# Kernel tuning notes

Measured on AMD Instinct MI355X. Metric: run time of the kernel, lower is better.

Reference implementation:

```python
import jax, jax.numpy as jnp
import numpy as np
from jax import lax

NUM_HEADS = 8
EMBED_DIM = 256
KEY_DIM = EMBED_DIM // NUM_HEADS  # 32


def rotate_every_two(x):
    x1 = x[..., ::2]
    x2 = x[..., 1::2]
    return jnp.stack((-x2, x1), axis=-1).reshape(x.shape)


def theta_shift(x, sin, cos):
    return x * cos + rotate_every_two(x) * sin


def setup_inputs() -> dict:
    key = jax.random.key(0)
    ks = jax.random.split(key, 16)
    b, H, W, E = 16, 64, 64, EMBED_DIM
    kd = KEY_DIM
    gain = 2 ** (-2.5)
    std_proj = gain * (2.0 / (E + E)) ** 0.5  # xavier_normal with gain
    std_out = (2.0 / (E + E)) ** 0.5
    return {
        "x": jax.random.normal(ks[0], (b, H, W, E), jnp.float32),
        "sin": jax.random.normal(ks[1], (H, W, kd), jnp.float32),
        "cos": jax.random.normal(ks[2], (H, W, kd), jnp.float32),
        "mask_h": jax.random.normal(ks[3], (NUM_HEADS, H, H), jnp.float32),
        "mask_w": jax.random.normal(ks[4], (NUM_HEADS, W, W), jnp.float32),
        "q_w": jax.random.normal(ks[5], (E, E), jnp.float32) * std_proj,
        "q_b": jnp.zeros((E,), jnp.float32),
        "k_w": jax.random.normal(ks[6], (E, E), jnp.float32) * std_proj,
        "k_b": jnp.zeros((E,), jnp.float32),
        "v_w": jax.random.normal(ks[7], (E, E), jnp.float32) * std_proj,
        "v_b": jnp.zeros((E,), jnp.float32),
        "lepe_w": jax.random.normal(ks[8], (5, 5, 1, E), jnp.float32) * 0.05,  # HWIO depthwise
        "lepe_b": jnp.zeros((E,), jnp.float32),
        "out_w": jax.random.normal(ks[9], (E, E), jnp.float32) * std_out,
        "out_b": jnp.zeros((E,), jnp.float32),
    }


def reference(x, sin, cos, mask_h, mask_w, q_w, q_b, k_w, k_b, v_w, v_b,
              lepe_w, lepe_b, out_w, out_b):
    b, H, W, E = x.shape
    nH, kd = NUM_HEADS, KEY_DIM
    vd = E // nH
    scaling = kd ** (-0.5)

    q = x @ q_w + q_b                       # [b,H,W,E]
    k = (x @ k_w + k_b) * scaling
    v = x @ v_w + v_b

    # depthwise 5x5 conv (lepe), NHWC
    lepe = lax.conv_general_dilated(
        v, lepe_w, window_strides=(1, 1), padding=[(2, 2), (2, 2)],
        dimension_numbers=("NHWC", "HWIO", "NHWC"), feature_group_count=E) + lepe_b

    q = q.reshape(b, H, W, nH, kd)
    k = k.reshape(b, H, W, nH, kd)
    v = v.reshape(b, H, W, nH, vd)

    sin_b = sin[:, :, None, :]              # [H,W,1,kd]
    cos_b = cos[:, :, None, :]
    qr = theta_shift(q, sin_b, cos_b)       # [b,H,W,nH,kd]
    kr = theta_shift(k, sin_b, cos_b)

    # width-wise attention: scores [b,H,nH,W,W]
    qk_w = jnp.einsum("bhqnd,bhknd->bhnqk", qr, kr)
    attn_w = jax.nn.softmax(qk_w + mask_w[None, None], axis=-1)
    v1 = jnp.einsum("bhnqk,bhknd->bhqnd", attn_w, v)  # [b,H,W,nH,vd]

    # height-wise attention: scores [b,W,nH,H,H]
    qk_h = jnp.einsum("bqwnd,bkwnd->bwnqk", qr, kr)
    attn_h = jax.nn.softmax(qk_h + mask_h[None, None], axis=-1)
    out = jnp.einsum("bwnqk,bkwnd->bqwnd", attn_h, v1)  # [b,H,W,nH,vd]

    out = out.reshape(b, H, W, E) + lepe
    return out @ out_w + out_b
```

## Files before the change

kernel.cpp:

```cpp
#include <hip/hip_runtime.h>

typedef unsigned short u16;
typedef __attribute__((ext_vector_type(4))) float f32x4;
typedef __attribute__((ext_vector_type(8))) short bf16x8;
typedef __attribute__((ext_vector_type(8))) u16 u16x8;
typedef __attribute__((ext_vector_type(4))) u16 u16x4v;

#define DI __device__ __forceinline__

DI u16 f2bf(float f) {
  unsigned int x = __float_as_uint(f);
  unsigned int r = (x + 0x7fffu + ((x >> 16) & 1u)) >> 16;
  return (u16)r;
}
DI float bf2f(u16 u) { return __uint_as_float(((unsigned int)u) << 16); }

__global__ __launch_bounds__(256) void pack_kernel(
    const float* __restrict__ qw, const float* __restrict__ qb,
    const float* __restrict__ kw, const float* __restrict__ kb,
    const float* __restrict__ vw, const float* __restrict__ vb,
    const float* __restrict__ ow,
    u16* __restrict__ wqkvT, float* __restrict__ bias, u16* __restrict__ owT)
{
  const int r = blockIdx.x;
  const int t = threadIdx.x;
  if (r < 768) {
    const int p = r >> 8, c = r & 255;
    const float* wsrc = p == 0 ? qw : (p == 1 ? kw : vw);
    const float sc = (p == 1) ? 0.17677669529663687f : 1.0f;
    wqkvT[r * 256 + t] = f2bf(wsrc[t * 256 + c] * sc);
    if (t == 0) {
      const float* bs = p == 0 ? qb : (p == 1 ? kb : vb);
      bias[r] = bs[c] * sc;
    }
  } else {
    const int c = r - 768;
    owT[c * 256 + t] = f2bf(ow[t * 256 + c]);
  }
}

__global__ __launch_bounds__(256, 2) void qkv_gemm_kernel(
    const float* __restrict__ x, const u16* __restrict__ wT, const float* __restrict__ bias,
    const float* __restrict__ sinp, const float* __restrict__ cosp,
    u16* __restrict__ qr, u16* __restrict__ kr, u16* __restrict__ v)
{
  __shared__ u16 As[32768];
  __shared__ float Tr[4][1024];
  const int t = threadIdx.x;
  const int wave = t >> 6, lane = t & 63;
  const int g = lane >> 4, lr = lane & 15;
  const int wr = wave >> 1, wc = wave & 1;
  const int m0 = blockIdx.x * 128;

  {
    char* Abw = (char*)As;
#pragma unroll
    for (int i = 0; i < 32; ++i) {
      const int c = t + 256 * i;
      const int row = c >> 6, cf = c & 63;
      const float4 xv = *reinterpret_cast<const float4*>(x + (m0 + row) * 256 + cf * 4);
      u16x4v bv;
      bv.x = f2bf(xv.x); bv.y = f2bf(xv.y); bv.z = f2bf(xv.z); bv.w = f2bf(xv.w);
      *reinterpret_cast<u16x4v*>(Abw + row * 512 + ((cf * 8) ^ ((row & 7) << 4))) = bv;
    }
  }
  __syncthreads();

  const char* Ab = (const char*)As;
  float* Trw = Tr[wave];
  const int tau = lane >> 3;
  const int kap = lane & 7;

  for (int cg = 0; cg < 6; ++cg) {
    const int c0 = cg * 128;
    f32x4 acc[4][4];
#pragma unroll
    for (int i = 0; i < 4; ++i)
#pragma unroll
      for (int j = 0; j < 4; ++j) acc[i][j] = (f32x4){0.f, 0.f, 0.f, 0.f};

#pragma unroll
    for (int ks = 0; ks < 8; ++ks) {
      bf16x8 af[4], bfr[4];
#pragma unroll
      for (int mt = 0; mt < 4; ++mt) {
        const int rr = wr * 64 + mt * 16 + lr;
        const int cb = (ks * 64 + g * 16) ^ ((rr & 7) << 4);
        af[mt] = *reinterpret_cast<const bf16x8*>(Ab + rr * 512 + cb);
      }
#pragma unroll
      for (int nt = 0; nt < 4; ++nt)
        bfr[nt] = *reinterpret_cast<const bf16x8*>(wT + (c0 + wc * 64 + nt * 16 + lr) * 256 + ks * 32 + g * 8);
#pragma unroll
      for (int mt = 0; mt < 4; ++mt)
#pragma unroll
        for (int nt = 0; nt < 4; ++nt)
          acc[mt][nt] = __builtin_amdgcn_mfma_f32_16x16x32_bf16(af[mt], bfr[nt], acc[mt][nt], 0, 0, 0);
    }

    const int colb = c0 + wc * 64;
    const int proj = colb >> 8;
    u16* dst = proj == 0 ? qr : (proj == 1 ? kr : v);
    const int e0 = (colb & 255) + kap * 8;

    float bcv[4];
#pragma unroll
    for (int nt = 0; nt < 4; ++nt) bcv[nt] = bias[colb + nt * 16 + lr];

#pragma unroll
    for (int mt = 0; mt < 4; ++mt) {
#pragma unroll
      for (int nt = 0; nt < 4; ++nt)
#pragma unroll
        for (int j = 0; j < 4; ++j)
          Trw[(g * 4 + j) * 64 + ((nt * 16 + lr) ^ (8 * j) ^ (16 * (g & 1)))] =
              acc[mt][nt][j] + bcv[nt];
      asm volatile("s_waitcnt lgkmcnt(0)" ::: "memory");
#pragma unroll
      for (int r2 = 0; r2 < 2; ++r2) {
        const int row = tau + 8 * r2;
        const int sig = (8 * (row & 3)) ^ (16 * ((row >> 2) & 1));
        const int rb = row * 64 + ((kap * 8) ^ sig);
        const float4 v0 = *reinterpret_cast<const float4*>(Trw + rb);
        const float4 v1 = *reinterpret_cast<const float4*>(Trw + rb + 4);
        const int tok = m0 + wr * 64 + mt * 16 + row;
        u16x8 o;
        if (proj < 2) {
          const int pos = tok & 4095;
          const int d0 = (kap * 8) & 31;
          const float* sp2 = sinp + pos * 32 + d0;
          const float* cp2 = cosp + pos * 32 + d0;
          {
            const float4 s0 = *reinterpret_cast<const float4*>(sp2);
            const float4 cA = *reinterpret_cast<const float4*>(cp2);
            o[0] = f2bf(v0.x * cA.x - v0.y * s0.x);
            o[1] = f2bf(v0.y * cA.y + v0.x * s0.y);
            o[2] = f2bf(v0.z * cA.z - v0.w * s0.z);
            o[3] = f2bf(v0.w * cA.w + v0.z * s0.w);
          }
          {
            const float4 s1 = *reinterpret_cast<const float4*>(sp2 + 4);
            const float4 cB = *reinterpret_cast<const float4*>(cp2 + 4);
            o[4] = f2bf(v1.x * cB.x - v1.y * s1.x);
            o[5] = f2bf(v1.y * cB.y + v1.x * s1.y);
            o[6] = f2bf(v1.z * cB.z - v1.w * s1.z);
            o[7] = f2bf(v1.w * cB.w + v1.z * s1.w);
          }
        } else {
          o[0] = f2bf(v0.x); o[1] = f2bf(v0.y); o[2] = f2bf(v0.z); o[3] = f2bf(v0.w);
          o[4] = f2bf(v1.x); o[5] = f2bf(v1.y); o[6] = f2bf(v1.z); o[7] = f2bf(v1.w);
        }
        *reinterpret_cast<u16x8*>(dst + tok * 256 + e0) = o;
      }
      asm volatile("s_waitcnt lgkmcnt(0)" ::: "memory");
    }
  }
}

__global__ __launch_bounds__(256, 2) void attn_kernel(
    const u16* __restrict__ qr, const u16* __restrict__ kr, const u16* __restrict__ vsrc,
    const float* __restrict__ mask, u16* __restrict__ dst, const int mode)
{
  __shared__ u16 Pbuf[4][64][72];
  __shared__ u16 Vt[256][80];
  const int t = threadIdx.x;
  const int wave = t >> 6, lane = t & 63;
  const int g = lane >> 4, lr = lane & 15;
  const int b = blockIdx.x >> 6, o = blockIdx.x & 63;
  const int base = (mode == 0) ? (b * 4096 + o * 64) * 256 : (b * 4096 + o) * 256;
  const int ts = (mode == 0) ? 256 : 16384;

#pragma unroll
  for (int i = 0; i < 8; ++i) {
    const int c = t + 256 * i;
    const int tok = c >> 5, ch = c & 31;
    const u16x8 val = *reinterpret_cast<const u16x8*>(vsrc + base + tok * ts + ch * 8);
    const int tc = tok ^ ((ch & 7) * 8);
#pragma unroll
    for (int j = 0; j < 8; ++j) Vt[ch * 8 + j][tc] = val[j];
  }
  __syncthreads();

  u16x4v obf[2][4][2];

  for (int hh = 0; hh < 2; ++hh) {
    const int n = wave * 2 + hh;
    bf16x8 qf[4], kf[4];
#pragma unroll
    for (int mt = 0; mt < 4; ++mt) {
      qf[mt] = *reinterpret_cast<const bf16x8*>(qr + base + (mt * 16 + lr) * ts + n * 32 + g * 8);
      kf[mt] = *reinterpret_cast<const bf16x8*>(kr + base + (mt * 16 + lr) * ts + n * 32 + g * 8);
    }
    const f32x4 zero = (f32x4){0.f, 0.f, 0.f, 0.f};
    f32x4 s[4][4];
#pragma unroll
    for (int mt = 0; mt < 4; ++mt)
#pragma unroll
      for (int nt = 0; nt < 4; ++nt)
        s[mt][nt] = __builtin_amdgcn_mfma_f32_16x16x32_bf16(qf[mt], kf[nt], zero, 0, 0, 0);

    const float* mp = mask + n * 4096;
#pragma unroll
    for (int mt = 0; mt < 4; ++mt) {
#pragma unroll
      for (int j = 0; j < 4; ++j) {
        const int r = mt * 16 + g * 4 + j;
#pragma unroll
        for (int nt = 0; nt < 4; ++nt)
          s[mt][nt][j] += mp[r * 64 + nt * 16 + lr];
        float m = fmaxf(fmaxf(s[mt][0][j], s[mt][1][j]), fmaxf(s[mt][2][j], s[mt][3][j]));
        m = fmaxf(m, __shfl_xor(m, 1));
        m = fmaxf(m, __shfl_xor(m, 2));
        m = fmaxf(m, __shfl_xor(m, 4));
        m = fmaxf(m, __shfl_xor(m, 8));
        float sum = 0.f;
#pragma unroll
        for (int nt = 0; nt < 4; ++nt) {
          const float p = __expf(s[mt][nt][j] - m);
          s[mt][nt][j] = p;
          sum += p;
        }
        sum += __shfl_xor(sum, 1);
        sum += __shfl_xor(sum, 2);
        sum += __shfl_xor(sum, 4);
        sum += __shfl_xor(sum, 8);
        const float rs = 1.f / sum;
#pragma unroll
        for (int nt = 0; nt < 4; ++nt)
          Pbuf[wave][r][nt * 16 + lr] = f2bf(s[mt][nt][j] * rs);
      }
    }

    f32x4 oacc[4][2];
#pragma unroll
    for (int mt = 0; mt < 4; ++mt)
#pragma unroll
      for (int nd = 0; nd < 2; ++nd) oacc[mt][nd] = zero;

#pragma unroll
    for (int kt = 0; kt < 2; ++kt) {
      bf16x8 pa[4];
#pragma unroll
      for (int mt = 0; mt < 4; ++mt)
        pa[mt] = *reinterpret_cast<const bf16x8*>(&Pbuf[wave][mt * 16 + lr][kt * 32 + g * 8]);
#pragma unroll
      for (int nd = 0; nd < 2; ++nd) {
        const int dcol = n * 32 + nd * 16 + lr;
        const bf16x8 vb = *reinterpret_cast<const bf16x8*>(
            &Vt[dcol][(kt * 32 + g * 8) ^ (((dcol >> 3) & 7) * 8)]);
#pragma unroll
        for (int mt = 0; mt < 4; ++mt)
          oacc[mt][nd] = __builtin_amdgcn_mfma_f32_16x16x32_bf16(vb, pa[mt], oacc[mt][nd], 0, 0, 0);
      }
    }
#pragma unroll
    for (int mt = 0; mt < 4; ++mt)
#pragma unroll
      for (int nd = 0; nd < 2; ++nd) {
        obf[hh][mt][nd].x = f2bf(oacc[mt][nd][0]);
        obf[hh][mt][nd].y = f2bf(oacc[mt][nd][1]);
        obf[hh][mt][nd].z = f2bf(oacc[mt][nd][2]);
        obf[hh][mt][nd].w = f2bf(oacc[mt][nd][3]);
      }
  }

  u16* Pw = &Pbuf[wave][0][0];
#pragma unroll
  for (int hh = 0; hh < 2; ++hh)
#pragma unroll
    for (int mt = 0; mt < 4; ++mt)
#pragma unroll
      for (int nd = 0; nd < 2; ++nd)
        *reinterpret_cast<u16x4v*>(Pw + (mt * 16 + lr) * 72 + hh * 32 + nd * 16 + g * 4) =
            obf[hh][mt][nd];
  asm volatile("s_waitcnt lgkmcnt(0)" ::: "memory");
#pragma unroll
  for (int r = 0; r < 8; ++r) {
    const int tok = r * 8 + (lane >> 3);
    const int ch = (lane & 7) * 8;
    const u16x8 val = *reinterpret_cast<const u16x8*>(Pw + tok * 72 + ch);
    *reinterpret_cast<u16x8*>(dst + base + tok * ts + wave * 64 + ch) = val;
  }
}

__global__ __launch_bounds__(256) void lepe_kernel(
    const u16* __restrict__ v, const float* __restrict__ cw, const float* __restrict__ cb,
    u16* __restrict__ lepe)
{
  const int t = threadIdx.x;
  const int cg = t & 31, pg = t >> 5;
  const int c0 = cg * 8;
  const int rowi = blockIdx.x >> 1;
  const int w0 = (blockIdx.x & 1) * 32 + pg * 4;
  const int h = rowi & 63;

  float acc[4][8];
#pragma unroll
  for (int p = 0; p < 4; ++p)
#pragma unroll
    for (int j = 0; j < 8; ++j) acc[p][j] = 0.f;

#pragma unroll
  for (int dy = 0; dy < 5; ++dy) {
    const int hh = h + dy - 2;
    if ((unsigned)hh >= 64u) continue;
    const u16* vrow = v + (size_t)(rowi + dy - 2) * 64 * 256 + c0;
    float fin[8][8];
#pragma unroll
    for (int i = 0; i < 8; ++i) {
      const int ww = w0 - 2 + i;
      if ((unsigned)ww < 64u) {
        const u16x8 val = *reinterpret_cast<const u16x8*>(vrow + ww * 256);
#pragma unroll
        for (int j = 0; j < 8; ++j) fin[i][j] = bf2f(val[j]);
      } else {
#pragma unroll
        for (int j = 0; j < 8; ++j) fin[i][j] = 0.f;
      }
    }
#pragma unroll
    for (int dx = 0; dx < 5; ++dx) {
      const float* wp = cw + (dy * 5 + dx) * 256 + c0;
      const float4 wA = *reinterpret_cast<const float4*>(wp);
      const float4 wB = *reinterpret_cast<const float4*>(wp + 4);
      const float wv[8] = {wA.x, wA.y, wA.z, wA.w, wB.x, wB.y, wB.z, wB.w};
#pragma unroll
      for (int p = 0; p < 4; ++p)
#pragma unroll
        for (int j = 0; j < 8; ++j)
          acc[p][j] += fin[p + dx][j] * wv[j];
    }
  }

#pragma unroll
  for (int p = 0; p < 4; ++p) {
    u16x8 r;
#pragma unroll
    for (int j = 0; j < 8; ++j) r[j] = f2bf(acc[p][j] + cb[c0 + j]);
    *reinterpret_cast<u16x8*>(lepe + ((size_t)rowi * 64 + w0 + p) * 256 + c0) = r;
  }
}

__global__ __launch_bounds__(256, 2) void out_gemm_kernel(
    const u16* __restrict__ ao, const u16* __restrict__ lep, const u16* __restrict__ owT,
    const float* __restrict__ ob, float* __restrict__ out)
{
  __shared__ u16 As[16384];
  const int t = threadIdx.x;
  const int wave = t >> 6, lane = t & 63;
  const int g = lane >> 4, lr = lane & 15;
  const int m0 = blockIdx.x * 64;

  char* Abw = (char*)As;
#pragma unroll
  for (int i = 0; i < 8; ++i) {
    const int c = t + 256 * i;
    const int row = c >> 5, bc = (c & 31) << 4;
    const int off = (m0 + row) * 256 + (c & 31) * 8;
    const u16x8 a = *reinterpret_cast<const u16x8*>(ao + off);
    const u16x8 l = *reinterpret_cast<const u16x8*>(lep + off);
    u16x8 s;
#pragma unroll
    for (int j = 0; j < 8; ++j) s[j] = f2bf(bf2f(a[j]) + bf2f(l[j]));
    *reinterpret_cast<u16x8*>(Abw + row * 512 + (bc ^ ((row & 7) << 4))) = s;
  }
  __syncthreads();

  const char* Ab = (const char*)As;
  for (int cg = 0; cg < 2; ++cg) {
    const int c0w = cg * 128 + wave * 32;
    f32x4 acc[4][2];
#pragma unroll
    for (int i = 0; i < 4; ++i)
#pragma unroll
      for (int j = 0; j < 2; ++j) acc[i][j] = (f32x4){0.f, 0.f, 0.f, 0.f};

#pragma unroll
    for (int ks = 0; ks < 8; ++ks) {
      bf16x8 af[4];
#pragma unroll
      for (int mt = 0; mt < 4; ++mt) {
        const int rr = mt * 16 + lr;
        const int cb = (ks * 64 + g * 16) ^ ((rr & 7) << 4);
        af[mt] = *reinterpret_cast<const bf16x8*>(Ab + rr * 512 + cb);
      }
#pragma unroll
      for (int nt = 0; nt < 2; ++nt) {
        const bf16x8 b =
            *reinterpret_cast<const bf16x8*>(owT + (c0w + nt * 16 + lr) * 256 + ks * 32 + g * 8);
#pragma unroll
        for (int mt = 0; mt < 4; ++mt)
          acc[mt][nt] = __builtin_amdgcn_mfma_f32_16x16x32_bf16(b, af[mt], acc[mt][nt], 0, 0, 0);
      }
    }

#pragma unroll
    for (int mt = 0; mt < 4; ++mt) {
      const int tok = m0 + mt * 16 + lr;
#pragma unroll
      for (int nt = 0; nt < 2; ++nt) {
        const int col0 = c0w + nt * 16 + g * 4;
        const float4 ob4 = *reinterpret_cast<const float4*>(ob + col0);
        float4 o;
        o.x = acc[mt][nt][0] + ob4.x;
        o.y = acc[mt][nt][1] + ob4.y;
        o.z = acc[mt][nt][2] + ob4.z;
        o.w = acc[mt][nt][3] + ob4.w;
        *reinterpret_cast<float4*>(out + tok * 256 + col0) = o;
      }
    }
  }
}

extern "C" void kernel_launch(void* const* d_in, const int* in_sizes, int n_in,
                              void* d_out, int out_size, void* d_ws, size_t ws_size,
                              hipStream_t stream)
{
  const float* x      = (const float*)d_in[0];
  const float* sinp   = (const float*)d_in[1];
  const float* cosp   = (const float*)d_in[2];
  const float* mask_h = (const float*)d_in[3];
  const float* mask_w = (const float*)d_in[4];
  const float* q_w    = (const float*)d_in[5];
  const float* q_b    = (const float*)d_in[6];
  const float* k_w    = (const float*)d_in[7];
  const float* k_b    = (const float*)d_in[8];
  const float* v_w    = (const float*)d_in[9];
  const float* v_b    = (const float*)d_in[10];
  const float* lepe_w = (const float*)d_in[11];
  const float* lepe_b = (const float*)d_in[12];
  const float* out_w  = (const float*)d_in[13];
  const float* out_b  = (const float*)d_in[14];

  unsigned char* ws = (unsigned char*)d_ws;
  const size_t SZ = 33554432;
  u16* qr    = (u16*)(ws);
  u16* kr    = (u16*)(ws + SZ);
  u16* vv    = (u16*)(ws + 2 * SZ);
  u16* v1    = (u16*)(ws + 3 * SZ);
  u16* lepe  = (u16*)(ws + 4 * SZ);
  u16* wqkvT = (u16*)(ws + 5 * SZ);
  u16* owT   = (u16*)(ws + 5 * SZ + 393216);
  float* bias = (float*)(ws + 5 * SZ + 393216 + 131072);
  u16* attn_out = vv;

  pack_kernel<<<1024, 256, 0, stream>>>(q_w, q_b, k_w, k_b, v_w, v_b, out_w, wqkvT, bias, owT);
  qkv_gemm_kernel<<<512, 256, 0, stream>>>(x, wqkvT, bias, sinp, cosp, qr, kr, vv);
  lepe_kernel<<<2048, 256, 0, stream>>>(vv, lepe_w, lepe_b, lepe);
  attn_kernel<<<1024, 256, 0, stream>>>(qr, kr, vv, mask_w, v1, 0);
  attn_kernel<<<1024, 256, 0, stream>>>(qr, kr, v1, mask_h, attn_out, 1);
  out_gemm_kernel<<<1024, 256, 0, stream>>>(attn_out, lepe, owT, out_b, (float*)d_out);
}
```

Baseline: 281.7 us.

## Compute transposed attention scores and pass probabilities via shuffles instead of LDS

The attention kernel now computes S^T (keys as rows) one 16-query tile at a time. Each query's softmax then reduces over a single lane column with two cross-lane shuffles, and the bf16 probabilities go straight into the P·V MFMA through 64-bit lane shuffles, so the per-wave LDS probability buffer is gone. The masks are pre-transposed in the pack kernel to match the new layout. The output staging reuses the V tile's shared memory with an XOR swizzle after a barrier, and launch bounds rise to 3 blocks per SU for more occupancy. The cost is extra shuffle instructions and more register pressure under the tighter bound.

```diff
diff --git a/kernel.cpp b/kernel.cpp
--- a/kernel.cpp
+++ b/kernel.cpp
@@ -1,10 +1,12 @@
 #include <hip/hip_runtime.h>
 
 typedef unsigned short u16;
+typedef unsigned long long u64;
 typedef __attribute__((ext_vector_type(4))) float f32x4;
 typedef __attribute__((ext_vector_type(8))) short bf16x8;
 typedef __attribute__((ext_vector_type(8))) u16 u16x8;
 typedef __attribute__((ext_vector_type(4))) u16 u16x4v;
+typedef __attribute__((ext_vector_type(2))) u64 u64x2;
 
 #define DI __device__ __forceinline__
 
@@ -14,13 +16,20 @@
   return (u16)r;
 }
 DI float bf2f(u16 u) { return __uint_as_float(((unsigned int)u) << 16); }
+DI u64 shfl64(u64 v, int src) {
+  int lo = __shfl((int)(unsigned int)(v & 0xffffffffu), src, 64);
+  int hi = __shfl((int)(unsigned int)(v >> 32), src, 64);
+  return ((u64)(unsigned int)hi << 32) | (u64)(unsigned int)lo;
+}
 
 __global__ __launch_bounds__(256) void pack_kernel(
     const float* __restrict__ qw, const float* __restrict__ qb,
     const float* __restrict__ kw, const float* __restrict__ kb,
     const float* __restrict__ vw, const float* __restrict__ vb,
     const float* __restrict__ ow,
-    u16* __restrict__ wqkvT, float* __restrict__ bias, u16* __restrict__ owT)
+    const float* __restrict__ mw, const float* __restrict__ mh,
+    u16* __restrict__ wqkvT, float* __restrict__ bias, u16* __restrict__ owT,
+    float* __restrict__ maskTw, float* __restrict__ maskTh)
 {
   const int r = blockIdx.x;
   const int t = threadIdx.x;
@@ -33,9 +42,18 @@
       const float* bs = p == 0 ? qb : (p == 1 ? kb : vb);
       bias[r] = bs[c] * sc;
     }
-  } else {
+  } else if (r < 1024) {
     const int c = r - 768;
     owT[c * 256 + t] = f2bf(ow[t * 256 + c]);
+  } else {
+    const int r2 = r - 1024;
+    const int sel = r2 >> 7;
+    const int n = (r2 >> 4) & 7;
+    const int k = (r2 & 15) * 4 + (t >> 6);
+    const int q = t & 63;
+    const float* msrc = sel ? mh : mw;
+    float* mdst = sel ? maskTh : maskTw;
+    mdst[(n * 64 + k) * 64 + q] = msrc[(n * 64 + q) * 64 + k];
   }
 }
 
@@ -157,11 +175,10 @@
   }
 }
 
-__global__ __launch_bounds__(256, 2) void attn_kernel(
+__global__ __launch_bounds__(256, 3) void attn_kernel(
     const u16* __restrict__ qr, const u16* __restrict__ kr, const u16* __restrict__ vsrc,
-    const float* __restrict__ mask, u16* __restrict__ dst, const int mode)
-{
-  __shared__ u16 Pbuf[4][64][72];
+    const float* __restrict__ maskT, u16* __restrict__ dst, const int mode)
+{
   __shared__ u16 Vt[256][80];
   const int t = threadIdx.x;
   const int wave = t >> 6, lane = t & 63;
@@ -182,104 +199,111 @@
   __syncthreads();
 
   u16x4v obf[2][4][2];
-
+  const f32x4 zero = (f32x4){0.f, 0.f, 0.f, 0.f};
+  const int srcA = (g & 1) * 32 + lr;
+  const int gg = g >> 1;
+
+#pragma unroll
   for (int hh = 0; hh < 2; ++hh) {
     const int n = wave * 2 + hh;
-    bf16x8 qf[4], kf[4];
-#pragma unroll
-    for (int mt = 0; mt < 4; ++mt) {
-      qf[mt] = *reinterpret_cast<const bf16x8*>(qr + base + (mt * 16 + lr) * ts + n * 32 + g * 8);
+    bf16x8 kf[4];
+#pragma unroll
+    for (int mt = 0; mt < 4; ++mt)
       kf[mt] = *reinterpret_cast<const bf16x8*>(kr + base + (mt * 16 + lr) * ts + n * 32 + g * 8);
-    }
-    const f32x4 zero = (f32x4){0.f, 0.f, 0.f, 0.f};
-    f32x4 s[4][4];
-#pragma unroll
-    for (int mt = 0; mt < 4; ++mt)
-#pragma unroll
-      for (int nt = 0; nt < 4; ++nt)
-        s[mt][nt] = __builtin_amdgcn_mfma_f32_16x16x32_bf16(qf[mt], kf[nt], zero, 0, 0, 0);
-
-    const float* mp = mask + n * 4096;
-#pragma unroll
-    for (int mt = 0; mt < 4; ++mt) {
-#pragma unroll
-      for (int j = 0; j < 4; ++j) {
-        const int r = mt * 16 + g * 4 + j;
-#pragma unroll
-        for (int nt = 0; nt < 4; ++nt)
-          s[mt][nt][j] += mp[r * 64 + nt * 16 + lr];
-        float m = fmaxf(fmaxf(s[mt][0][j], s[mt][1][j]), fmaxf(s[mt][2][j], s[mt][3][j]));
-        m = fmaxf(m, __shfl_xor(m, 1));
-        m = fmaxf(m, __shfl_xor(m, 2));
-        m = fmaxf(m, __shfl_xor(m, 4));
-        m = fmaxf(m, __shfl_xor(m, 8));
-        float sum = 0.f;
-#pragma unroll
-        for (int nt = 0; nt < 4; ++nt) {
-          const float p = __expf(s[mt][nt][j] - m);
-          s[mt][nt][j] = p;
+    const float* mp = maskT + n * 4096;
+
+#pragma unroll
+    for (int qmt = 0; qmt < 4; ++qmt) {
+      const bf16x8 qf =
+          *reinterpret_cast<const bf16x8*>(qr + base + (qmt * 16 + lr) * ts + n * 32 + g * 8);
+      f32x4 st[4];
+#pragma unroll
+      for (int kmt = 0; kmt < 4; ++kmt)
+        st[kmt] = __builtin_amdgcn_mfma_f32_16x16x32_bf16(kf[kmt], qf, zero, 0, 0, 0);
+#pragma unroll
+      for (int kmt = 0; kmt < 4; ++kmt)
+#pragma unroll
+        for (int j = 0; j < 4; ++j)
+          st[kmt][j] += mp[(kmt * 16 + g * 4 + j) * 64 + qmt * 16 + lr];
+
+      float mx = st[0][0];
+#pragma unroll
+      for (int kmt = 0; kmt < 4; ++kmt)
+#pragma unroll
+        for (int j = 0; j < 4; ++j) mx = fmaxf(mx, st[kmt][j]);
+      mx = fmaxf(mx, __shfl_xor(mx, 16));
+      mx = fmaxf(mx, __shfl_xor(mx, 32));
+      float sum = 0.f;
+#pragma unroll
+      for (int kmt = 0; kmt < 4; ++kmt)
+#pragma unroll
+        for (int j = 0; j < 4; ++j) {
+          const float p = __expf(st[kmt][j] - mx);
+          st[kmt][j] = p;
           sum += p;
         }
-        sum += __shfl_xor(sum, 1);
-        sum += __shfl_xor(sum, 2);
-        sum += __shfl_xor(sum, 4);
-        sum += __shfl_xor(sum, 8);
-        const float rs = 1.f / sum;
-#pragma unroll
-        for (int nt = 0; nt < 4; ++nt)
-          Pbuf[wave][r][nt * 16 + lr] = f2bf(s[mt][nt][j] * rs);
-      }
-    }
-
-    f32x4 oacc[4][2];
-#pragma unroll
-    for (int mt = 0; mt < 4; ++mt)
-#pragma unroll
-      for (int nd = 0; nd < 2; ++nd) oacc[mt][nd] = zero;
-
-#pragma unroll
-    for (int kt = 0; kt < 2; ++kt) {
-      bf16x8 pa[4];
-#pragma unroll
-      for (int mt = 0; mt < 4; ++mt)
-        pa[mt] = *reinterpret_cast<const bf16x8*>(&Pbuf[wave][mt * 16 + lr][kt * 32 + g * 8]);
+      sum += __shfl_xor(sum, 16);
+      sum += __shfl_xor(sum, 32);
+      const float rs = 1.f / sum;
+      u64 p64[4];
+#pragma unroll
+      for (int kmt = 0; kmt < 4; ++kmt) {
+        const u64 a0 = f2bf(st[kmt][0] * rs);
+        const u64 a1 = f2bf(st[kmt][1] * rs);
+        const u64 a2 = f2bf(st[kmt][2] * rs);
+        const u64 a3 = f2bf(st[kmt][3] * rs);
+        p64[kmt] = a0 | (a1 << 16) | (a2 << 32) | (a3 << 48);
+      }
+
+      f32x4 oacc[2];
+      oacc[0] = zero; oacc[1] = zero;
+#pragma unroll
+      for (int kt = 0; kt < 2; ++kt) {
+        const u64 lo0 = shfl64(p64[2 * kt + 0], srcA);
+        const u64 lo1 = shfl64(p64[2 * kt + 1], srcA);
+        const u64 hi0 = shfl64(p64[2 * kt + 0], srcA + 16);
+        const u64 hi1 = shfl64(p64[2 * kt + 1], srcA + 16);
+        u64x2 qq;
+        qq.x = gg ? lo1 : lo0;
+        qq.y = gg ? hi1 : hi0;
+        const bf16x8 pb = *reinterpret_cast<const bf16x8*>(&qq);
+#pragma unroll
+        for (int nd = 0; nd < 2; ++nd) {
+          const int dcol = n * 32 + nd * 16 + lr;
+          const bf16x8 vb = *reinterpret_cast<const bf16x8*>(
+              &Vt[dcol][(kt * 32 + g * 8) ^ (((dcol >> 3) & 7) * 8)]);
+          oacc[nd] = __builtin_amdgcn_mfma_f32_16x16x32_bf16(vb, pb, oacc[nd], 0, 0, 0);
+        }
+      }
 #pragma unroll
       for (int nd = 0; nd < 2; ++nd) {
-        const int dcol = n * 32 + nd * 16 + lr;
-        const bf16x8 vb = *reinterpret_cast<const bf16x8*>(
-            &Vt[dcol][(kt * 32 + g * 8) ^ (((dcol >> 3) & 7) * 8)]);
-#pragma unroll
-        for (int mt = 0; mt < 4; ++mt)
-          oacc[mt][nd] = __builtin_amdgcn_mfma_f32_16x16x32_bf16(vb, pa[mt], oacc[mt][nd], 0, 0, 0);
-      }
-    }
-#pragma unroll
-    for (int mt = 0; mt < 4; ++mt)
+        obf[hh][qmt][nd].x = f2bf(oacc[nd][0]);
+        obf[hh][qmt][nd].y = f2bf(oacc[nd][1]);
+        obf[hh][qmt][nd].z = f2bf(oacc[nd][2]);
+        obf[hh][qmt][nd].w = f2bf(oacc[nd][3]);
+      }
+    }
+  }
+
+  __syncthreads();
+  u16* Ow = &Vt[0][0] + wave * 4608;
+#pragma unroll
+  for (int hh = 0; hh < 2; ++hh)
+#pragma unroll
+    for (int qmt = 0; qmt < 4; ++qmt)
 #pragma unroll
       for (int nd = 0; nd < 2; ++nd) {
-        obf[hh][mt][nd].x = f2bf(oacc[mt][nd][0]);
-        obf[hh][mt][nd].y = f2bf(oacc[mt][nd][1]);
-        obf[hh][mt][nd].z = f2bf(oacc[mt][nd][2]);
-        obf[hh][mt][nd].w = f2bf(oacc[mt][nd][3]);
-      }
-  }
-
-  u16* Pw = &Pbuf[wave][0][0];
-#pragma unroll
-  for (int hh = 0; hh < 2; ++hh)
-#pragma unroll
-    for (int mt = 0; mt < 4; ++mt)
-#pragma unroll
-      for (int nd = 0; nd < 2; ++nd)
-        *reinterpret_cast<u16x4v*>(Pw + (mt * 16 + lr) * 72 + hh * 32 + nd * 16 + g * 4) =
-            obf[hh][mt][nd];
+        const int tokl = qmt * 16 + lr;
+        const int col = hh * 32 + nd * 16 + g * 4;
+        *reinterpret_cast<u16x4v*>(Ow + tokl * 72 + (col ^ ((tokl & 7) * 8))) = obf[hh][qmt][nd];
+      }
   asm volatile("s_waitcnt lgkmcnt(0)" ::: "memory");
 #pragma unroll
   for (int r = 0; r < 8; ++r) {
-    const int tok = r * 8 + (lane >> 3);
-    const int ch = (lane & 7) * 8;
-    const u16x8 val = *reinterpret_cast<const u16x8*>(Pw + tok * 72 + ch);
-    *reinterpret_cast<u16x8*>(dst + base + tok * ts + wave * 64 + ch) = val;
+    const int tokl = r * 8 + (lane >> 3);
+    const int kap = lane & 7;
+    const u16x8 val = *reinterpret_cast<const u16x8*>(Ow + tokl * 72 + ((kap ^ (tokl & 7)) * 8));
+    *reinterpret_cast<u16x8*>(dst + base + tokl * ts + wave * 64 + kap * 8) = val;
   }
 }
 
@@ -441,13 +465,16 @@
   u16* lepe  = (u16*)(ws + 4 * SZ);
   u16* wqkvT = (u16*)(ws + 5 * SZ);
   u16* owT   = (u16*)(ws + 5 * SZ + 393216);
-  float* bias = (float*)(ws + 5 * SZ + 393216 + 131072);
+  float* bias   = (float*)(ws + 5 * SZ + 524288);
+  float* maskTw = (float*)(ws + 5 * SZ + 528384);
+  float* maskTh = (float*)(ws + 5 * SZ + 659456);
   u16* attn_out = vv;
 
-  pack_kernel<<<1024, 256, 0, stream>>>(q_w, q_b, k_w, k_b, v_w, v_b, out_w, wqkvT, bias, owT);
+  pack_kernel<<<1280, 256, 0, stream>>>(q_w, q_b, k_w, k_b, v_w, v_b, out_w,
+                                        mask_w, mask_h, wqkvT, bias, owT, maskTw, maskTh);
   qkv_gemm_kernel<<<512, 256, 0, stream>>>(x, wqkvT, bias, sinp, cosp, qr, kr, vv);
   lepe_kernel<<<2048, 256, 0, stream>>>(vv, lepe_w, lepe_b, lepe);
-  attn_kernel<<<1024, 256, 0, stream>>>(qr, kr, vv, mask_w, v1, 0);
-  attn_kernel<<<1024, 256, 0, stream>>>(qr, kr, v1, mask_h, attn_out, 1);
+  attn_kernel<<<1024, 256, 0, stream>>>(qr, kr, vv, maskTw, v1, 0);
+  attn_kernel<<<1024, 256, 0, stream>>>(qr, kr, v1, maskTh, attn_out, 1);
   out_gemm_kernel<<<1024, 256, 0, stream>>>(attn_out, lepe, owT, out_b, (float*)d_out);
 }
```

Result: slower. 340.8 us (+21.0%).
